# Optimization experiments

Hardware: AMD Instinct MI355X
Metric: run time of the kernel (lower is better)

Reference implementation:

```python
import jax, jax.numpy as jnp
import numpy as np

B, S, D, Q, U = 32, 8192, 256, 256, 128


def setup_inputs() -> dict:
    key = jax.random.key(0)
    k1, k2, k3, k4, k5 = jax.random.split(key, 5)
    query = jax.random.normal(k1, (B, Q), dtype=jnp.float32)
    values = jax.random.normal(k2, (B, S, D), dtype=jnp.float32)
    # Dense kernels (Keras stores as [in, out]); scale ~ Glorot-ish
    W1 = jax.random.normal(k3, (D, U), dtype=jnp.float32) * 0.05
    W2 = jax.random.normal(k4, (Q, U), dtype=jnp.float32) * 0.05
    V = jax.random.normal(k5, (U, 1), dtype=jnp.float32) * 0.05
    return {"query": query, "values": values, "W1": W1, "W2": W2, "V": V}


def reference(query, values, W1, W2, V):
    # score = V^T tanh(W1*values + W2*query)  -> (B, S, 1)
    proj_v = jnp.einsum('bsd,du->bsu', values, W1)          # (B,S,U)
    proj_q = jnp.einsum('bq,qu->bu', query, W2)[:, None, :]  # (B,1,U)
    score = jnp.einsum('bsu,uo->bso', jnp.tanh(proj_v + proj_q), V)  # (B,S,1)
    attention_weights = jax.nn.softmax(score, axis=1)        # softmax over seq_len
    # dropout is identity at inference (training=False)
    context = jnp.sum(attention_weights * values, axis=1)    # (B,D)
    return context, attention_weights
```

## Files before the change

kernel.cpp:

```cpp
#include <hip/hip_runtime.h>
#include <stdint.h>

#define B_ 32
#define S_ 8192
#define D_ 256
#define Q_ 256
#define U_ 128
#define NCHUNK 64
#define LSTR 72

typedef float floatx4 __attribute__((ext_vector_type(4)));
typedef float f32x4 __attribute__((ext_vector_type(4)));
typedef __bf16 bf16x8 __attribute__((ext_vector_type(8)));
typedef unsigned short ushortx4 __attribute__((ext_vector_type(4)));
typedef unsigned short ushortx8 __attribute__((ext_vector_type(8)));

static __device__ __forceinline__ unsigned short f2bf(float f) {
    unsigned int x = __builtin_bit_cast(unsigned int, f);
    x += 0x7FFFu + ((x >> 16) & 1u);
    return (unsigned short)(x >> 16);
}

static __device__ __forceinline__ float fast_tanh(float x) {
    x = fminf(15.f, fmaxf(-15.f, x));
    float e = __expf(2.f * x);
    return __fdividef(e - 1.f, e + 1.f);
}

__global__ __launch_bounds__(128) void prep_kernel(
        const float* __restrict__ query, const float* __restrict__ W1,
        const float* __restrict__ W2, float* __restrict__ pq,
        unsigned short* __restrict__ w1t) {
    int b = blockIdx.x;
    int t = threadIdx.x;
    __shared__ float qrow[Q_];
    qrow[t] = query[b * Q_ + t];
    qrow[t + 128] = query[b * Q_ + 128 + t];
    __syncthreads();
    float acc = 0.f;
#pragma unroll 8
    for (int q = 0; q < Q_; ++q) acc = fmaf(qrow[q], W2[q * U_ + t], acc);
    pq[b * U_ + t] = acc;
    int base = (b * 128 + t) * 8;
#pragma unroll
    for (int j = 0; j < 8; ++j) {
        int e = base + j;
        int n = e >> 8, k = e & 255;
        w1t[e] = f2bf(W1[k * U_ + n]);
    }
}

__global__ __launch_bounds__(256, 4) void fused_kernel(
        const float* __restrict__ values, const unsigned short* __restrict__ w1t,
        const float* __restrict__ pq, const float* __restrict__ V,
        float* __restrict__ scores, float* __restrict__ mbuf,
        float* __restrict__ lbuf, float* __restrict__ cpart) {
    __shared__ __align__(16) char smem[2 * 128 * LSTR * 2];
    unsigned short* As = (unsigned short*)smem;
    unsigned short* Bs = As + 128 * LSTR;
    float* part = (float*)smem;
    float* sarr = part + 256;
    float* parr = sarr + 128;
    float* redm = parr + 128;
    floatx4* cbuf = (floatx4*)(smem + 4096);

    int b = blockIdx.y;
    int cid = blockIdx.x;
    int s0 = cid * 128;
    int tid = threadIdx.x;
    int lane = tid & 63;
    int wave = tid >> 6;
    int wr = wave >> 1, wc = wave & 1;
    int cc = lane & 15, qg = lane >> 4;

    const float* vb = values + ((size_t)b * S_ + s0) * D_;

    f32x4 acc[4][4];
#pragma unroll
    for (int mt = 0; mt < 4; ++mt)
#pragma unroll
        for (int nt = 0; nt < 4; ++nt) acc[mt][nt] = (f32x4){0.f, 0.f, 0.f, 0.f};

    int arow = tid >> 4, ac = tid & 15;
    int brow = tid >> 3, bc = tid & 7;

    for (int kt = 0; kt < 4; ++kt) {
        int k0 = kt * 64;
        __syncthreads();
#pragma unroll
        for (int i = 0; i < 8; ++i) {
            int row = arow + i * 16;
            floatx4 v = *reinterpret_cast<const floatx4*>(vb + (size_t)row * D_ + k0 + ac * 4);
            ushortx4 u;
            u[0] = f2bf(v[0]); u[1] = f2bf(v[1]); u[2] = f2bf(v[2]); u[3] = f2bf(v[3]);
            *reinterpret_cast<ushortx4*>(&As[row * LSTR + ac * 4]) = u;
        }
#pragma unroll
        for (int i = 0; i < 4; ++i) {
            int row = brow + i * 32;
            ushortx8 w = *reinterpret_cast<const ushortx8*>(&w1t[row * 256 + k0 + bc * 8]);
            *reinterpret_cast<ushortx8*>(&Bs[row * LSTR + bc * 8]) = w;
        }
        __syncthreads();
#pragma unroll
        for (int ks = 0; ks < 2; ++ks) {
            bf16x8 af[4], bfr[4];
#pragma unroll
            for (int mt = 0; mt < 4; ++mt)
                af[mt] = *reinterpret_cast<const bf16x8*>(
                    &As[(wr * 64 + mt * 16 + cc) * LSTR + ks * 32 + qg * 8]);
#pragma unroll
            for (int nt = 0; nt < 4; ++nt)
                bfr[nt] = *reinterpret_cast<const bf16x8*>(
                    &Bs[(wc * 64 + nt * 16 + cc) * LSTR + ks * 32 + qg * 8]);
#pragma unroll
            for (int mt = 0; mt < 4; ++mt)
#pragma unroll
                for (int nt = 0; nt < 4; ++nt)
                    acc[mt][nt] = __builtin_amdgcn_mfma_f32_16x16x32_bf16(
                        af[mt], bfr[nt], acc[mt][nt], 0, 0, 0);
        }
    }
    __syncthreads();

    float Vu[4], pqu[4];
#pragma unroll
    for (int nt = 0; nt < 4; ++nt) {
        int u = wc * 64 + nt * 16 + cc;
        Vu[nt] = V[u];
        pqu[nt] = pq[b * U_ + u];
    }
#pragma unroll
    for (int mt = 0; mt < 4; ++mt) {
#pragma unroll
        for (int r = 0; r < 4; ++r) {
            float s = 0.f;
#pragma unroll
            for (int nt = 0; nt < 4; ++nt)
                s += Vu[nt] * fast_tanh(acc[mt][nt][r] + pqu[nt]);
            s += __shfl_xor(s, 1);
            s += __shfl_xor(s, 2);
            s += __shfl_xor(s, 4);
            s += __shfl_xor(s, 8);
            if (cc == 0) part[wc * 128 + wr * 64 + mt * 16 + qg * 4 + r] = s;
        }
    }
    __syncthreads();
    if (tid < 128) {
        float sc = part[tid] + part[128 + tid];
        scores[(size_t)b * S_ + s0 + tid] = sc;
        sarr[tid] = sc;
    }
    __syncthreads();
    if (tid < 64) {
        float m = fmaxf(sarr[tid], sarr[tid + 64]);
#pragma unroll
        for (int off = 32; off >= 1; off >>= 1) m = fmaxf(m, __shfl_xor(m, off));
        if (tid == 0) redm[0] = m;
    }
    __syncthreads();
    float M = redm[0];
    if (tid < 128) parr[tid] = __expf(sarr[tid] - M);
    __syncthreads();
    if (tid < 64) {
        float l = parr[tid] + parr[tid + 64];
#pragma unroll
        for (int off = 32; off >= 1; off >>= 1) l += __shfl_xor(l, off);
        if (tid == 0) { mbuf[b * NCHUNK + cid] = M; lbuf[b * NCHUNK + cid] = l; }
    }

    int g = tid & 63, sub = tid >> 6;
    floatx4 acc4 = {0.f, 0.f, 0.f, 0.f};
#pragma unroll 4
    for (int i = 0; i < 32; ++i) {
        int r = i * 4 + sub;
        float w = parr[r];
        floatx4 v = *reinterpret_cast<const floatx4*>(vb + (size_t)r * D_ + g * 4);
        acc4 += v * w;
    }
    cbuf[tid] = acc4;
    __syncthreads();
    if (tid < 64) {
        floatx4 r4 = cbuf[tid] + cbuf[tid + 64] + cbuf[tid + 128] + cbuf[tid + 192];
        *reinterpret_cast<floatx4*>(cpart + ((size_t)b * NCHUNK + cid) * D_ + g * 4) = r4;
    }
}

__global__ __launch_bounds__(256) void finalize_kernel(
        const float* __restrict__ scores, const float* __restrict__ mbuf,
        const float* __restrict__ lbuf, const float* __restrict__ cpart,
        float* __restrict__ out) {
    int b = blockIdx.x;
    int part_id = blockIdx.y;
    int tid = threadIdx.x;
    __shared__ float MZ[2];
    __shared__ float alpha[NCHUNK];
    if (tid < 64) {
        float m = mbuf[b * NCHUNK + tid];
        float l = lbuf[b * NCHUNK + tid];
        float M = m;
#pragma unroll
        for (int off = 32; off >= 1; off >>= 1) M = fmaxf(M, __shfl_xor(M, off));
        float z = l * __expf(m - M);
#pragma unroll
        for (int off = 32; off >= 1; off >>= 1) z += __shfl_xor(z, off);
        if (tid == 0) { MZ[0] = M; MZ[1] = z; }
    }
    __syncthreads();
    float M = MZ[0];
    float invZ = 1.f / MZ[1];

    if (part_id < 8) {
        size_t off = (size_t)b * S_ + part_id * 1024;
        floatx4 v = *reinterpret_cast<const floatx4*>(scores + off + tid * 4);
        floatx4 w;
#pragma unroll
        for (int j = 0; j < 4; ++j) w[j] = __expf(v[j] - M) * invZ;
        *reinterpret_cast<floatx4*>(out + B_ * D_ + off + tid * 4) = w;
    } else {
        if (tid < 64) alpha[tid] = __expf(mbuf[b * NCHUNK + tid] - M) * invZ;
        __syncthreads();
        float acc = 0.f;
#pragma unroll 8
        for (int c = 0; c < NCHUNK; ++c)
            acc = fmaf(alpha[c], cpart[((size_t)b * NCHUNK + c) * D_ + tid], acc);
        out[b * D_ + tid] = acc;
    }
}

extern "C" void kernel_launch(void* const* d_in, const int* in_sizes, int n_in,
                              void* d_out, int out_size, void* d_ws, size_t ws_size,
                              hipStream_t stream) {
    const float* query  = (const float*)d_in[0];
    const float* values = (const float*)d_in[1];
    const float* W1     = (const float*)d_in[2];
    const float* W2     = (const float*)d_in[3];
    const float* V      = (const float*)d_in[4];
    float* out = (float*)d_out;

    char* ws = (char*)d_ws;
    unsigned short* w1t = (unsigned short*)ws;               ws += 65536;
    float* pq     = (float*)ws;                              ws += 16384;
    float* scores = (float*)ws;                              ws += B_ * S_ * 4;
    float* mbuf   = (float*)ws;                              ws += B_ * NCHUNK * 4;
    float* lbuf   = (float*)ws;                              ws += B_ * NCHUNK * 4;
    float* cpart  = (float*)ws;

    prep_kernel<<<dim3(32), dim3(128), 0, stream>>>(query, W1, W2, pq, w1t);
    fused_kernel<<<dim3(NCHUNK, B_), dim3(256), 0, stream>>>(values, w1t, pq, V,
                                                             scores, mbuf, lbuf, cpart);
    finalize_kernel<<<dim3(B_, 9), dim3(256), 0, stream>>>(scores, mbuf, lbuf, cpart, out);
}
```

Measured before the change: 419.3 us.

## Stage full bf16 values tile in LDS and reuse it for context sum

Loads the whole 128x256 values tile once into shared memory as bf16, using an XOR swizzle in place of padding, and streams only W1 slices per k-step. The context accumulation then reads values from LDS as bf16 instead of reloading fp32 values from global memory, which removes the second global read of the values tile. In exchange, shared memory grows to 80KB, occupancy drops from 4 to 2 blocks per CU, and the context sum now uses bf16-rounded values, which loses precision.

```diff
diff --git a/kernel.cpp b/kernel.cpp
--- a/kernel.cpp
+++ b/kernel.cpp
@@ -7,7 +7,6 @@
 #define Q_ 256
 #define U_ 128
 #define NCHUNK 64
-#define LSTR 72
 
 typedef float floatx4 __attribute__((ext_vector_type(4)));
 typedef float f32x4 __attribute__((ext_vector_type(4)));
@@ -19,6 +18,11 @@
     unsigned int x = __builtin_bit_cast(unsigned int, f);
     x += 0x7FFFu + ((x >> 16) & 1u);
     return (unsigned short)(x >> 16);
+}
+
+static __device__ __forceinline__ float bf2f(unsigned short u) {
+    unsigned int x = ((unsigned int)u) << 16;
+    return __builtin_bit_cast(float, x);
 }
 
 static __device__ __forceinline__ float fast_tanh(float x) {
@@ -50,19 +54,19 @@
     }
 }
 
-__global__ __launch_bounds__(256, 4) void fused_kernel(
+__global__ __launch_bounds__(256, 2) void fused_kernel(
         const float* __restrict__ values, const unsigned short* __restrict__ w1t,
         const float* __restrict__ pq, const float* __restrict__ V,
         float* __restrict__ scores, float* __restrict__ mbuf,
         float* __restrict__ lbuf, float* __restrict__ cpart) {
-    __shared__ __align__(16) char smem[2 * 128 * LSTR * 2];
+    __shared__ __align__(16) char smem[81920];
     unsigned short* As = (unsigned short*)smem;
-    unsigned short* Bs = As + 128 * LSTR;
-    float* part = (float*)smem;
+    unsigned short* Bs = (unsigned short*)(smem + 65536);
+    float* part = (float*)(smem + 65536);
     float* sarr = part + 256;
     float* parr = sarr + 128;
     float* redm = parr + 128;
-    floatx4* cbuf = (floatx4*)(smem + 4096);
+    floatx4* cbuf = (floatx4*)(smem + 65536 + 4096);
 
     int b = blockIdx.y;
     int cid = blockIdx.x;
@@ -72,6 +76,7 @@
     int wave = tid >> 6;
     int wr = wave >> 1, wc = wave & 1;
     int cc = lane & 15, qg = lane >> 4;
+    int cc7 = cc & 7;
 
     const float* vb = values + ((size_t)b * S_ + s0) * D_;
 
@@ -81,38 +86,42 @@
 #pragma unroll
         for (int nt = 0; nt < 4; ++nt) acc[mt][nt] = (f32x4){0.f, 0.f, 0.f, 0.f};
 
-    int arow = tid >> 4, ac = tid & 15;
-    int brow = tid >> 3, bc = tid & 7;
+#pragma unroll
+    for (int i = 0; i < 32; ++i) {
+        int fidx = tid + i * 256;
+        int row = fidx >> 6, fc = fidx & 63;
+        floatx4 v = *reinterpret_cast<const floatx4*>(vb + (size_t)row * D_ + fc * 4);
+        ushortx4 u;
+        u[0] = f2bf(v[0]); u[1] = f2bf(v[1]); u[2] = f2bf(v[2]); u[3] = f2bf(v[3]);
+        int addr = row * 256 + (((fc >> 1) ^ (row & 7)) << 3) + (fc & 1) * 4;
+        *reinterpret_cast<ushortx4*>(&As[addr]) = u;
+    }
+#pragma unroll
+    for (int i = 0; i < 4; ++i) {
+        int cidx = tid + i * 256;
+        int n = cidx >> 3, kc = cidx & 7;
+        ushortx8 w = *reinterpret_cast<const ushortx8*>(&w1t[n * 256 + kc * 8]);
+        *reinterpret_cast<ushortx8*>(&Bs[n * 64 + ((kc ^ (n & 7)) << 3)]) = w;
+    }
+    __syncthreads();
 
     for (int kt = 0; kt < 4; ++kt) {
-        int k0 = kt * 64;
-        __syncthreads();
-#pragma unroll
-        for (int i = 0; i < 8; ++i) {
-            int row = arow + i * 16;
-            floatx4 v = *reinterpret_cast<const floatx4*>(vb + (size_t)row * D_ + k0 + ac * 4);
-            ushortx4 u;
-            u[0] = f2bf(v[0]); u[1] = f2bf(v[1]); u[2] = f2bf(v[2]); u[3] = f2bf(v[3]);
-            *reinterpret_cast<ushortx4*>(&As[row * LSTR + ac * 4]) = u;
-        }
-#pragma unroll
-        for (int i = 0; i < 4; ++i) {
-            int row = brow + i * 32;
-            ushortx8 w = *reinterpret_cast<const ushortx8*>(&w1t[row * 256 + k0 + bc * 8]);
-            *reinterpret_cast<ushortx8*>(&Bs[row * LSTR + bc * 8]) = w;
-        }
-        __syncthreads();
 #pragma unroll
         for (int ks = 0; ks < 2; ++ks) {
+            int ksg = kt * 2 + ks;
             bf16x8 af[4], bfr[4];
 #pragma unroll
-            for (int mt = 0; mt < 4; ++mt)
+            for (int mt = 0; mt < 4; ++mt) {
+                int r = wr * 64 + mt * 16 + cc;
                 af[mt] = *reinterpret_cast<const bf16x8*>(
-                    &As[(wr * 64 + mt * 16 + cc) * LSTR + ks * 32 + qg * 8]);
-#pragma unroll
-            for (int nt = 0; nt < 4; ++nt)
+                    &As[r * 256 + (((ksg * 4 + qg) ^ cc7) << 3)]);
+            }
+#pragma unroll
+            for (int nt = 0; nt < 4; ++nt) {
+                int n = wc * 64 + nt * 16 + cc;
                 bfr[nt] = *reinterpret_cast<const bf16x8*>(
-                    &Bs[(wc * 64 + nt * 16 + cc) * LSTR + ks * 32 + qg * 8]);
+                    &Bs[n * 64 + (((ks * 4 + qg) ^ cc7) << 3)]);
+            }
 #pragma unroll
             for (int mt = 0; mt < 4; ++mt)
 #pragma unroll
@@ -120,8 +129,20 @@
                     acc[mt][nt] = __builtin_amdgcn_mfma_f32_16x16x32_bf16(
                         af[mt], bfr[nt], acc[mt][nt], 0, 0, 0);
         }
-    }
-    __syncthreads();
+        __syncthreads();
+        if (kt < 3) {
+            int kt1 = kt + 1;
+#pragma unroll
+            for (int i = 0; i < 4; ++i) {
+                int cidx = tid + i * 256;
+                int n = cidx >> 3, kc = cidx & 7;
+                ushortx8 w = *reinterpret_cast<const ushortx8*>(
+                    &w1t[n * 256 + kt1 * 64 + kc * 8]);
+                *reinterpret_cast<ushortx8*>(&Bs[n * 64 + ((kc ^ (n & 7)) << 3)]) = w;
+            }
+            __syncthreads();
+        }
+    }
 
     float Vu[4], pqu[4];
 #pragma unroll
@@ -168,6 +189,7 @@
         for (int off = 32; off >= 1; off >>= 1) l += __shfl_xor(l, off);
         if (tid == 0) { mbuf[b * NCHUNK + cid] = M; lbuf[b * NCHUNK + cid] = l; }
     }
+    __syncthreads();
 
     int g = tid & 63, sub = tid >> 6;
     floatx4 acc4 = {0.f, 0.f, 0.f, 0.f};
@@ -175,8 +197,12 @@
     for (int i = 0; i < 32; ++i) {
         int r = i * 4 + sub;
         float w = parr[r];
-        floatx4 v = *reinterpret_cast<const floatx4*>(vb + (size_t)r * D_ + g * 4);
-        acc4 += v * w;
+        int addr = r * 256 + (((g >> 1) ^ (r & 7)) << 3) + (g & 1) * 4;
+        ushortx4 u = *reinterpret_cast<const ushortx4*>(&As[addr]);
+        acc4[0] = fmaf(bf2f(u[0]), w, acc4[0]);
+        acc4[1] = fmaf(bf2f(u[1]), w, acc4[1]);
+        acc4[2] = fmaf(bf2f(u[2]), w, acc4[2]);
+        acc4[3] = fmaf(bf2f(u[3]), w, acc4[3]);
     }
     cbuf[tid] = acc4;
     __syncthreads();
```

Result: no change. 417.3 us (-0.5%).
